# Performance work log

Measured on AMD Instinct MI355X. Metric: run time of the kernel, lower is better.

Reference implementation:

```python
import jax, jax.numpy as jnp
import numpy as np

B, T, H = 4096, 512, 256


def setup_inputs() -> dict:
    key = jax.random.key(0)
    ks = jax.random.split(key, 10)
    s = 0.05
    return {
        "x": jax.random.normal(ks[0], (B, T, 1), dtype=jnp.float32),
        "eps": jax.random.normal(ks[1], (B, T, 1), dtype=jnp.float32),  # randn_like noise, pregenerated
        "w_ih": jax.random.normal(ks[2], (4 * H, 1), dtype=jnp.float32) * s,
        "w_hh": jax.random.normal(ks[3], (4 * H, H), dtype=jnp.float32) * s,
        "b_ih": jax.random.normal(ks[4], (4 * H,), dtype=jnp.float32) * s,
        "b_hh": jax.random.normal(ks[5], (4 * H,), dtype=jnp.float32) * s,
        "w_mean": jax.random.normal(ks[6], (1, H), dtype=jnp.float32) * s,
        "b_mean": jax.random.normal(ks[7], (1,), dtype=jnp.float32) * s,
        "w_logvar": jax.random.normal(ks[8], (1, H), dtype=jnp.float32) * s,
        "b_logvar": jax.random.normal(ks[9], (1,), dtype=jnp.float32) * s,
    }


def reference(x, eps, w_ih, w_hh, b_ih, b_hh, w_mean, b_mean, w_logvar, b_logvar):
    """Teacher-forcing forward: per-step LSTMCell + mean/logvar heads + reparam sample.
    Returns (outputs, means, logvars), each [B, T, 1]."""
    b = x.shape[0]
    h0 = jnp.zeros((b, H), dtype=x.dtype)
    c0 = jnp.zeros((b, H), dtype=x.dtype)

    def step(carry, inp):
        h, c = carry
        xt, et = inp  # [B,1] each
        # PyTorch LSTMCell: gates ordered (i, f, g, o)
        gates = xt @ w_ih.T + b_ih + h @ w_hh.T + b_hh  # [B, 4H]
        i, f, g, o = jnp.split(gates, 4, axis=-1)
        i = jax.nn.sigmoid(i)
        f = jax.nn.sigmoid(f)
        g = jnp.tanh(g)
        o = jax.nn.sigmoid(o)
        c = f * c + i * g
        h = o * jnp.tanh(c)
        mean = h @ w_mean.T + b_mean            # [B, 1]
        logvar = jnp.clip(h @ w_logvar.T + b_logvar, -10.0, 2.0)
        sample = mean + jnp.exp(0.5 * logvar) * et
        return (h, c), (sample, mean, logvar)

    xs = (jnp.swapaxes(x, 0, 1), jnp.swapaxes(eps, 0, 1))  # time-major [T,B,1]
    _, (s, m, lv) = jax.lax.scan(step, (h0, c0), xs)
    to_bt = lambda a: jnp.swapaxes(a, 0, 1)  # back to [B,T,1]
    return to_bt(s), to_bt(m), to_bt(lv)
```

## Files before the change

### kernel.cpp

```cpp
#include <hip/hip_runtime.h>
#include <hip/hip_bf16.h>

#define BB 4096
#define TT 512
#define HH 256

typedef __bf16 bf16x8 __attribute__((ext_vector_type(8)));
typedef __bf16 bf16x4 __attribute__((ext_vector_type(4)));
typedef float f32x4 __attribute__((ext_vector_type(4)));
typedef long fp8frag;

#define MFMA_BF16 __builtin_amdgcn_mfma_f32_16x16x32_bf16
#define MFMA_FP8  __builtin_amdgcn_mfma_f32_16x16x32_fp8_fp8

#if defined(__has_builtin)
#if __has_builtin(__builtin_amdgcn_exp2f)
#define EXP2F(x) __builtin_amdgcn_exp2f(x)
#endif
#endif
#ifndef EXP2F
#define EXP2F(x) __expf((x) * 0.6931471805599453f)
#endif
#define RCPF(x) __builtin_amdgcn_rcpf(x)

#define L2E  1.4426950408889634f
#define TL2E 2.8853900817779268f
#define HL2E 0.7213475204444817f

__global__ void prep_weights8(const float* __restrict__ w_hh, const float* __restrict__ w_ih,
                              const float* __restrict__ b_ih, const float* __restrict__ b_hh,
                              char* __restrict__ wB8) {
    int idx = blockIdx.x * blockDim.x + threadIdx.x;
    if (idx >= 64 * 9 * 64) return;
    int l = idx & 63;
    int kt = (idx >> 6) % 9;
    int ctg = idx / (9 * 64);
    int n = ctg * 16 + (l & 15);
    int k0 = kt * 32 + 8 * (l >> 4);
    float f[8];
#pragma unroll
    for (int e = 0; e < 8; ++e) {
        int k = k0 + e;
        float v = 0.f;
        if (k < 256) v = w_hh[n * HH + k];
        else if (k == 256) v = w_ih[n];
        else if (k == 257) v = b_ih[n] + b_hh[n];
        f[e] = v * 64.f;
    }
    int lo = __builtin_amdgcn_cvt_pk_fp8_f32(f[0], f[1], 0, false);
    lo = __builtin_amdgcn_cvt_pk_fp8_f32(f[2], f[3], lo, true);
    int hi = __builtin_amdgcn_cvt_pk_fp8_f32(f[4], f[5], 0, false);
    hi = __builtin_amdgcn_cvt_pk_fp8_f32(f[6], f[7], hi, true);
    int2 v; v.x = lo; v.y = hi;
    *(int2*)(wB8 + (size_t)idx * 8) = v;
}

#define SGg(v) RCPF(1.f + EXP2F(-(v)))
#define THg(v) (1.f - 2.f * RCPF(EXP2F(v) + 1.f))

__global__ __launch_bounds__(512, 1) void lstm_fused(
    const float* __restrict__ x, const float* __restrict__ eps,
    const float* __restrict__ w_mean, const float* __restrict__ b_mean,
    const float* __restrict__ w_logvar, const float* __restrict__ b_logvar,
    const char* __restrict__ wB8, float* __restrict__ out)
{
    __shared__ __align__(16) char wlds8[8][18][512];
    __shared__ __align__(16) __bf16 hbuf[2][16][296];
    __shared__ __align__(16) char hbuf8[2][16][296];
    __shared__ __align__(16) __bf16 headw[9][512];
    __shared__ float obuf[2][16][16];

    const int tid = threadIdx.x;
    const int w = tid >> 6;
    const int l = tid & 63;
    const int m0 = blockIdx.x * 16;

    for (int i = tid; i < 2 * 16 * 296; i += 512) (&hbuf[0][0][0])[i] = (__bf16)0.f;
    for (int i = tid; i < 2 * 16 * 296; i += 512) (&hbuf8[0][0][0])[i] = 0;
    for (int i = tid; i < 9 * 64; i += 512) {
        int kt = i >> 6, hl = i & 63;
        int col = hl & 15;
        int k0 = kt * 32 + 8 * (hl >> 4);
        bf16x8 hw;
#pragma unroll
        for (int e = 0; e < 8; ++e) {
            int k = k0 + e;
            float v = 0.f;
            if (k < 256) {
                if (col == 0) v = w_mean[k];
                else if (col == 1) v = w_logvar[k];
            } else if (k == 257) {
                if (col == 0) v = b_mean[0];
                else if (col == 1) v = b_logvar[0];
            }
            hw[e] = (__bf16)v;
        }
        *(bf16x8*)&headw[kt][hl * 8] = hw;
    }

    fp8frag wreg8[45];
#pragma unroll
    for (int kt = 0; kt < 9; ++kt) {
        wreg8[kt]      = *(const fp8frag*)(wB8 + ((size_t)((w)      * 9 + kt) * 64 + l) * 8);
        wreg8[9 + kt]  = *(const fp8frag*)(wB8 + ((size_t)((w + 16) * 9 + kt) * 64 + l) * 8);
        wreg8[18 + kt] = *(const fp8frag*)(wB8 + ((size_t)((w + 8)  * 9 + kt) * 64 + l) * 8);
        wreg8[27 + kt] = *(const fp8frag*)(wB8 + ((size_t)((w + 24) * 9 + kt) * 64 + l) * 8);
        wreg8[36 + kt] = *(const fp8frag*)(wB8 + ((size_t)((w + 40) * 9 + kt) * 64 + l) * 8);
        *(fp8frag*)&wlds8[w][kt][l * 8] =
            *(const fp8frag*)(wB8 + ((size_t)((w + 32) * 9 + kt) * 64 + l) * 8);
        *(fp8frag*)&wlds8[w][9 + kt][l * 8] =
            *(const fp8frag*)(wB8 + ((size_t)((w + 48) * 9 + kt) * 64 + l) * 8);
    }
    const char* pc7 = wB8 + ((size_t)((w + 56) * 9 + 4) * 64 + l) * 8;

    const int arow = l & 15;
    const int ako = 8 * (l >> 4);
    const int u0 = 16 * w + ((l >> 4) << 2);
    const int u1 = u0 + 128;

    const float DS1c = L2E / 1024.f;
    const float DS2c = TL2E / 1024.f;

    float c[8];
#pragma unroll
    for (int i = 0; i < 8; ++i) c[i] = 0.f;
    const f32x4 Z = {0.f, 0.f, 0.f, 0.f};

    __syncthreads();
    if (tid < 16) {
        hbuf[0][tid][257] = (__bf16)1.0f;
        hbuf[1][tid][257] = (__bf16)1.0f;
        hbuf8[0][tid][257] = (char)__builtin_amdgcn_cvt_pk_fp8_f32(16.f, 0.f, 0, false);
        hbuf8[1][tid][257] = (char)__builtin_amdgcn_cvt_pk_fp8_f32(16.f, 0.f, 0, false);
        float x0 = x[(size_t)(m0 + tid) * TT];
        hbuf[1][tid][256] = (__bf16)x0;
        hbuf8[1][tid][256] = (char)__builtin_amdgcn_cvt_pk_fp8_f32(x0 * 16.f, 0.f, 0, false);
    }
    fp8frag sbf = *(const fp8frag*)(pc7 - 2048);
    fp8frag tbf;
    __syncthreads();

#define P0KT(KT)                                                                \
    do {                                                                        \
        a0 = MFMA_FP8(wreg8[KT], hf[KT], (KT) ? a0 : Z, 0, 0, 0);               \
        a1 = MFMA_FP8(wreg8[9 + (KT)], hf[KT], (KT) ? a1 : Z, 0, 0, 0);         \
        a2 = MFMA_FP8(*(const fp8frag*)&wlds8[w][KT][l * 8], hf[KT], (KT) ? a2 : Z, 0, 0, 0);       \
        a3 = MFMA_FP8(*(const fp8frag*)&wlds8[w][9 + (KT)][l * 8], hf[KT], (KT) ? a3 : Z, 0, 0, 0); \
    } while (0)

#define P1KT(KT, NXT, USE, PF)                                                  \
    do {                                                                        \
        PF = *(const fp8frag*)(pc7 + ((NXT) - 4) * 512);                        \
        a4 = MFMA_FP8(wreg8[18 + (KT)], hf[KT], (KT) ? a4 : Z, 0, 0, 0);        \
        a5 = MFMA_FP8(wreg8[27 + (KT)], hf[KT], (KT) ? a5 : Z, 0, 0, 0);        \
        a6 = MFMA_FP8(wreg8[36 + (KT)], hf[KT], (KT) ? a6 : Z, 0, 0, 0);        \
        a7 = MFMA_FP8(USE, hf[KT], (KT) ? a7 : Z, 0, 0, 0);                     \
    } while (0)

#define EWP0C(J)                                                                \
    do {                                                                        \
        float gi_ = a0[J] * DS1c, gf_ = a1[J] * DS1c;                           \
        float gg_ = a2[J] * DS2c, go_ = a3[J] * DS1c;                           \
        float cn_ = fmaf(SGg(gf_), c[J], SGg(gi_) * THg(gg_));                  \
        c[J] = cn_;                                                             \
        hA[J] = SGg(go_) * THg(cn_ * TL2E);                                     \
    } while (0)

#define EWP1C(J)                                                                \
    do {                                                                        \
        float gi_ = a4[J] * DS1c, gf_ = a5[J] * DS1c;                           \
        float gg_ = a6[J] * DS2c, go_ = a7[J] * DS1c;                           \
        float cn_ = fmaf(SGg(gf_), c[4 + (J)], SGg(gi_) * THg(gg_));            \
        c[4 + (J)] = cn_;                                                       \
        hB[J] = SGg(go_) * THg(cn_ * TL2E);                                     \
    } while (0)

#define WRH(PB, HV, U)                                                          \
    do {                                                                        \
        bf16x4 hb_ = {(__bf16)HV[0], (__bf16)HV[1], (__bf16)HV[2], (__bf16)HV[3]};\
        *(bf16x4*)&hbuf[PB][arow][U] = hb_;                                     \
        int pk_ = __builtin_amdgcn_cvt_pk_fp8_f32(HV[0] * 16.f, HV[1] * 16.f, 0, false);\
        pk_ = __builtin_amdgcn_cvt_pk_fp8_f32(HV[2] * 16.f, HV[3] * 16.f, pk_, true);  \
        *(int*)&hbuf8[PB][arow][U] = pk_;                                       \
    } while (0)

#define HEADS(RB, SLOT)                                                         \
    do {                                                                        \
        f32x4 ah_;                                                              \
        {                                                                       \
            bf16x8 hb_ = *(const bf16x8*)&hbuf[RB][arow][0 * 32 + ako];         \
            ah_ = MFMA_BF16(*(const bf16x8*)&headw[0][l * 8], hb_, Z, 0, 0, 0); \
        }                                                                       \
        _Pragma("unroll")                                                       \
        for (int kt_ = 1; kt_ < 9; ++kt_) {                                     \
            bf16x8 hb_ = *(const bf16x8*)&hbuf[RB][arow][kt_ * 32 + ako];       \
            ah_ = MFMA_BF16(*(const bf16x8*)&headw[kt_][l * 8], hb_, ah_, 0, 0, 0);\
        }                                                                       \
        if (l < 16) {                                                           \
            obuf[0][l][SLOT] = ah_[0];                                          \
            obuf[1][l][SLOT] = fminf(fmaxf(ah_[1], -10.f), 2.f);                \
        }                                                                       \
    } while (0)

#define FLUSH(T0)                                                               \
    do {                                                                        \
        if (tid < 192) {                                                        \
            const int o_ = tid >> 6, rr_ = (tid >> 2) & 15, q_ = tid & 3;       \
            f32x4 mv_ = *(const f32x4*)&obuf[0][rr_][q_ * 4];                   \
            f32x4 lv_ = *(const f32x4*)&obuf[1][rr_][q_ * 4];                   \
            const size_t base_ = (size_t)(m0 + rr_) * TT + (T0) + q_ * 4;       \
            if (o_ == 0) {                                                      \
                f32x4 e_ = *(const f32x4*)&eps[base_];                          \
                f32x4 s_;                                                       \
                _Pragma("unroll")                                               \
                for (int k_ = 0; k_ < 4; ++k_)                                  \
                    s_[k_] = fmaf(EXP2F(lv_[k_] * HL2E), e_[k_], mv_[k_]);      \
                *(f32x4*)&out[base_] = s_;                                      \
            } else if (o_ == 1) {                                               \
                *(f32x4*)&out[(size_t)BB * TT + base_] = mv_;                   \
            } else {                                                            \
                *(f32x4*)&out[2 * (size_t)BB * TT + base_] = lv_;               \
            }                                                                   \
        }                                                                       \
    } while (0)

#define STEP(PB, RB, BA, BX)                                                    \
    do {                                                                        \
        const int tt = t0 + (PB);                                               \
        float xn = 0.f;                                                         \
        if (tid < 16 && tt + 1 < TT) xn = x[(size_t)(m0 + tid) * TT + (tt + 1)];\
        fp8frag hf[9];                                                          \
        _Pragma("unroll")                                                       \
        for (int kt_ = 0; kt_ < 9; ++kt_)                                       \
            hf[kt_] = *(const fp8frag*)&hbuf8[RB][arow][kt_ * 32 + ako];        \
        f32x4 a0, a1, a2, a3, a4, a5, a6, a7;                                   \
        float hA[4], hB[4];                                                     \
        P0KT(0); P0KT(1); P0KT(2); P0KT(3); P0KT(4);                            \
        P0KT(5); P0KT(6); P0KT(7); P0KT(8);                                     \
        P1KT(0, 1, BA, BX); P1KT(1, 2, BX, BA); EWP0C(0);                       \
        P1KT(2, 3, BA, BX); P1KT(3, 4, BX, BA); EWP0C(1);                       \
        P1KT(4, 5, BA, BX); P1KT(5, 6, BX, BA); EWP0C(2);                       \
        P1KT(6, 7, BA, BX); P1KT(7, 8, BX, BA); EWP0C(3);                       \
        P1KT(8, 0, BA, BX);                                                     \
        WRH(PB, hA, u0);                                                        \
        if (w == 7 && tt >= 1) { HEADS(RB, (tt - 1) & 15); }                    \
        EWP1C(0); EWP1C(1); EWP1C(2); EWP1C(3);                                 \
        WRH(PB, hB, u1);                                                        \
        if (tid < 16 && tt + 1 < TT) {                                          \
            hbuf[PB][tid][256] = (__bf16)xn;                                    \
            hbuf8[PB][tid][256] =                                               \
                (char)__builtin_amdgcn_cvt_pk_fp8_f32(xn * 16.f, 0.f, 0, false);\
        }                                                                       \
        if ((PB) == 0 && tt > 0 && (tt & 15) == 0) {                            \
            __syncthreads();                                                    \
            FLUSH(tt - 16);                                                     \
        }                                                                       \
        __syncthreads();                                                        \
    } while (0)

    for (int t0 = 0; t0 < TT; t0 += 2) {
        STEP(0, 1, sbf, tbf);
        STEP(1, 0, tbf, sbf);
    }

    if (w == 7) { HEADS(1, 15); }
    __syncthreads();
    FLUSH(TT - 16);

#undef P0KT
#undef P1KT
#undef EWP0C
#undef EWP1C
#undef WRH
#undef HEADS
#undef FLUSH
#undef STEP
}

extern "C" void kernel_launch(void* const* d_in, const int* in_sizes, int n_in,
                              void* d_out, int out_size, void* d_ws, size_t ws_size,
                              hipStream_t stream) {
    const float* x = (const float*)d_in[0];
    const float* eps = (const float*)d_in[1];
    const float* w_ih = (const float*)d_in[2];
    const float* w_hh = (const float*)d_in[3];
    const float* b_ih = (const float*)d_in[4];
    const float* b_hh = (const float*)d_in[5];
    const float* w_mean = (const float*)d_in[6];
    const float* b_mean = (const float*)d_in[7];
    const float* w_logvar = (const float*)d_in[8];
    const float* b_logvar = (const float*)d_in[9];

    char* wB8 = (char*)d_ws;

    prep_weights8<<<144, 256, 0, stream>>>(w_hh, w_ih, b_ih, b_hh, wB8);
    lstm_fused<<<256, 512, 0, stream>>>(x, eps, w_mean, b_mean, w_logvar, b_logvar,
                                        wB8, (float*)d_out);
}
```

Before: 1.077 ms.

## Defer second-half gate elementwise to next step to overlap with MFMA

```diff
diff --git a/kernel.cpp b/kernel.cpp
--- a/kernel.cpp
+++ b/kernel.cpp
@@ -125,6 +125,7 @@
 #pragma unroll
     for (int i = 0; i < 8; ++i) c[i] = 0.f;
     const f32x4 Z = {0.f, 0.f, 0.f, 0.f};
+    f32x4 sa4 = Z, sa5 = Z, sa6 = Z, sa7 = Z;
 
     __syncthreads();
     if (tid < 16) {
@@ -157,7 +158,7 @@
         a7 = MFMA_FP8(USE, hf[KT], (KT) ? a7 : Z, 0, 0, 0);                     \
     } while (0)
 
-#define EWP0C(J)                                                                \
+#define EWAC(J)                                                                 \
     do {                                                                        \
         float gi_ = a0[J] * DS1c, gf_ = a1[J] * DS1c;                           \
         float gg_ = a2[J] * DS2c, go_ = a3[J] * DS1c;                           \
@@ -166,10 +167,10 @@
         hA[J] = SGg(go_) * THg(cn_ * TL2E);                                     \
     } while (0)
 
-#define EWP1C(J)                                                                \
-    do {                                                                        \
-        float gi_ = a4[J] * DS1c, gf_ = a5[J] * DS1c;                           \
-        float gg_ = a6[J] * DS2c, go_ = a7[J] * DS1c;                           \
+#define EWBC(J)                                                                 \
+    do {                                                                        \
+        float gi_ = sa4[J] * DS1c, gf_ = sa5[J] * DS1c;                         \
+        float gg_ = sa6[J] * DS2c, go_ = sa7[J] * DS1c;                         \
         float cn_ = fmaf(SGg(gf_), c[4 + (J)], SGg(gi_) * THg(gg_));            \
         c[4 + (J)] = cn_;                                                       \
         hB[J] = SGg(go_) * THg(cn_ * TL2E);                                     \
@@ -184,21 +185,33 @@
         *(int*)&hbuf8[PB][arow][U] = pk_;                                       \
     } while (0)
 
-#define HEADS(RB, SLOT)                                                         \
-    do {                                                                        \
-        f32x4 ah_;                                                              \
-        {                                                                       \
-            bf16x8 hb_ = *(const bf16x8*)&hbuf[RB][arow][0 * 32 + ako];         \
-            ah_ = MFMA_BF16(*(const bf16x8*)&headw[0][l * 8], hb_, Z, 0, 0, 0); \
-        }                                                                       \
-        _Pragma("unroll")                                                       \
-        for (int kt_ = 1; kt_ < 9; ++kt_) {                                     \
-            bf16x8 hb_ = *(const bf16x8*)&hbuf[RB][arow][kt_ * 32 + ako];       \
-            ah_ = MFMA_BF16(*(const bf16x8*)&headw[kt_][l * 8], hb_, ah_, 0, 0, 0);\
-        }                                                                       \
+#define HP1(RB)                                                                 \
+    do {                                                                        \
+        bf16x8 hb_ = *(const bf16x8*)&hbuf[RB][arow][0 * 32 + ako];             \
+        ahh = MFMA_BF16(*(const bf16x8*)&headw[0][l * 8], hb_, Z, 0, 0, 0);     \
+        hb_ = *(const bf16x8*)&hbuf[RB][arow][1 * 32 + ako];                    \
+        ahh = MFMA_BF16(*(const bf16x8*)&headw[1][l * 8], hb_, ahh, 0, 0, 0);   \
+        hb_ = *(const bf16x8*)&hbuf[RB][arow][2 * 32 + ako];                    \
+        ahh = MFMA_BF16(*(const bf16x8*)&headw[2][l * 8], hb_, ahh, 0, 0, 0);   \
+        hb_ = *(const bf16x8*)&hbuf[RB][arow][3 * 32 + ako];                    \
+        ahh = MFMA_BF16(*(const bf16x8*)&headw[3][l * 8], hb_, ahh, 0, 0, 0);   \
+        hb_ = *(const bf16x8*)&hbuf[RB][arow][8 * 32 + ako];                    \
+        ahh = MFMA_BF16(*(const bf16x8*)&headw[8][l * 8], hb_, ahh, 0, 0, 0);   \
+    } while (0)
+
+#define HP2(RB, SLOT)                                                           \
+    do {                                                                        \
+        bf16x8 hb_ = *(const bf16x8*)&hbuf[RB][arow][4 * 32 + ako];             \
+        ahh = MFMA_BF16(*(const bf16x8*)&headw[4][l * 8], hb_, ahh, 0, 0, 0);   \
+        hb_ = *(const bf16x8*)&hbuf[RB][arow][5 * 32 + ako];                    \
+        ahh = MFMA_BF16(*(const bf16x8*)&headw[5][l * 8], hb_, ahh, 0, 0, 0);   \
+        hb_ = *(const bf16x8*)&hbuf[RB][arow][6 * 32 + ako];                    \
+        ahh = MFMA_BF16(*(const bf16x8*)&headw[6][l * 8], hb_, ahh, 0, 0, 0);   \
+        hb_ = *(const bf16x8*)&hbuf[RB][arow][7 * 32 + ako];                    \
+        ahh = MFMA_BF16(*(const bf16x8*)&headw[7][l * 8], hb_, ahh, 0, 0, 0);   \
         if (l < 16) {                                                           \
-            obuf[0][l][SLOT] = ah_[0];                                          \
-            obuf[1][l][SLOT] = fminf(fmaxf(ah_[1], -10.f), 2.f);                \
+            obuf[0][l][SLOT] = ahh[0];                                          \
+            obuf[1][l][SLOT] = fminf(fmaxf(ahh[1], -10.f), 2.f);                \
         }                                                                       \
     } while (0)
 
@@ -230,22 +243,39 @@
         float xn = 0.f;                                                         \
         if (tid < 16 && tt + 1 < TT) xn = x[(size_t)(m0 + tid) * TT + (tt + 1)];\
         fp8frag hf[9];                                                          \
-        _Pragma("unroll")                                                       \
-        for (int kt_ = 0; kt_ < 9; ++kt_)                                       \
-            hf[kt_] = *(const fp8frag*)&hbuf8[RB][arow][kt_ * 32 + ako];        \
-        f32x4 a0, a1, a2, a3, a4, a5, a6, a7;                                   \
+        hf[0] = *(const fp8frag*)&hbuf8[RB][arow][0 * 32 + ako];                \
+        hf[1] = *(const fp8frag*)&hbuf8[RB][arow][1 * 32 + ako];                \
+        hf[2] = *(const fp8frag*)&hbuf8[RB][arow][2 * 32 + ako];                \
+        hf[3] = *(const fp8frag*)&hbuf8[RB][arow][3 * 32 + ako];                \
+        hf[8] = *(const fp8frag*)&hbuf8[RB][arow][8 * 32 + ako];                \
+        f32x4 a0, a1, a2, a3, a4, a5, a6, a7, ahh;                              \
         float hA[4], hB[4];                                                     \
-        P0KT(0); P0KT(1); P0KT(2); P0KT(3); P0KT(4);                            \
-        P0KT(5); P0KT(6); P0KT(7); P0KT(8);                                     \
-        P1KT(0, 1, BA, BX); P1KT(1, 2, BX, BA); EWP0C(0);                       \
-        P1KT(2, 3, BA, BX); P1KT(3, 4, BX, BA); EWP0C(1);                       \
-        P1KT(4, 5, BA, BX); P1KT(5, 6, BX, BA); EWP0C(2);                       \
-        P1KT(6, 7, BA, BX); P1KT(7, 8, BX, BA); EWP0C(3);                       \
-        P1KT(8, 0, BA, BX);                                                     \
+         \
+        P0KT(0); P1KT(0, 1, BA, BX);                                            \
+        if (tt > 0) EWBC(0);                                                    \
+        P0KT(1); P1KT(1, 2, BX, BA);                                            \
+        if (tt > 0) EWBC(1);                                                    \
+        P0KT(2); P1KT(2, 3, BA, BX);                                            \
+        if (tt > 0) EWBC(2);                                                    \
+        P0KT(3); P1KT(3, 8, BX, BA);                                            \
+        if (tt > 0) EWBC(3);                                                    \
+        P0KT(8); P1KT(8, 4, BA, BX);                                            \
+        if (w == 7 && tt >= 1) HP1(RB);                                         \
+        if (tt > 0) WRH(RB, hB, u1);                                            \
+        __syncthreads();                                                        \
+         \
+        hf[4] = *(const fp8frag*)&hbuf8[RB][arow][4 * 32 + ako];                \
+        hf[5] = *(const fp8frag*)&hbuf8[RB][arow][5 * 32 + ako];                \
+        hf[6] = *(const fp8frag*)&hbuf8[RB][arow][6 * 32 + ako];                \
+        hf[7] = *(const fp8frag*)&hbuf8[RB][arow][7 * 32 + ako];                \
+        P0KT(4); P0KT(5); P0KT(6); P0KT(7);                                     \
+        if (w == 7 && tt >= 1) HP2(RB, (tt - 1) & 15);                          \
+        P1KT(4, 5, BX, BA); EWAC(0);                                            \
+        P1KT(5, 6, BA, BX); EWAC(1);                                            \
+        P1KT(6, 7, BX, BA); EWAC(2);                                            \
+        P1KT(7, 0, BA, BX); EWAC(3);                                            \
+        sa4 = a4; sa5 = a5; sa6 = a6; sa7 = a7;                                 \
         WRH(PB, hA, u0);                                                        \
-        if (w == 7 && tt >= 1) { HEADS(RB, (tt - 1) & 15); }                    \
-        EWP1C(0); EWP1C(1); EWP1C(2); EWP1C(3);                                 \
-        WRH(PB, hB, u1);                                                        \
         if (tid < 16 && tt + 1 < TT) {                                          \
             hbuf[PB][tid][256] = (__bf16)xn;                                    \
             hbuf8[PB][tid][256] =                                               \
@@ -263,16 +293,27 @@
         STEP(1, 0, tbf, sbf);
     }
 
-    if (w == 7) { HEADS(1, 15); }
-    __syncthreads();
-    FLUSH(TT - 16);
+    {
+        float hB[4];
+        EWBC(0); EWBC(1); EWBC(2); EWBC(3);
+        WRH(1, hB, u1);
+        __syncthreads();
+        if (w == 7) {
+            f32x4 ahh;
+            HP1(1);
+            HP2(1, 15);
+        }
+        __syncthreads();
+        FLUSH(TT - 16);
+    }
 
 #undef P0KT
 #undef P1KT
-#undef EWP0C
-#undef EWP1C
+#undef EWAC
+#undef EWBC
 #undef WRH
-#undef HEADS
+#undef HP1
+#undef HP2
 #undef FLUSH
 #undef STEP
 }
```

New measurement: 1.076 ms. No clear change (-0.1%).
